# Optimization experiments

Hardware: AMD Instinct MI355X
Metric: run time of the kernel (lower is better)

Reference implementation:

```python
import jax, jax.numpy as jnp
import numpy as np

B, T, F, H, C = 128, 2048, 2, 64, 2
EPS = 1e-5  # BatchNorm eps (eval mode, running stats)


def setup_inputs() -> dict:
    key = jax.random.key(0)
    ks = jax.random.split(key, 23)
    rn = lambda k, s, sc=0.1: jax.random.normal(k, s, jnp.float32) * sc
    return {
        "x": jax.random.normal(ks[0], (B, T, F), jnp.float32),
        "tags": jax.random.randint(ks[1], (B, T), 0, C),
        "cw1": rn(ks[2], (H, F)), "cb1": rn(ks[3], (H,)),
        "cwr": rn(ks[4], (3, H, H)), "cbr": rn(ks[5], (3, H)),
        "bn_g": 1.0 + rn(ks[6], (4, H)), "bn_b": rn(ks[7], (4, H)),
        "bn_m": rn(ks[8], (4, H)),
        "bn_v": 0.5 + jax.random.uniform(ks[9], (4, H), jnp.float32),
        "wih_f": rn(ks[10], (4 * H, H)), "whh_f": rn(ks[11], (4 * H, H)),
        "bih_f": rn(ks[12], (4 * H,)), "bhh_f": rn(ks[13], (4 * H,)),
        "wih_b": rn(ks[14], (4 * H, H)), "whh_b": rn(ks[15], (4 * H, H)),
        "bih_b": rn(ks[16], (4 * H,)), "bhh_b": rn(ks[17], (4 * H,)),
        "fc_w": rn(ks[18], (C, 2 * H)), "fc_b": rn(ks[19], (C,)),
        "crf_start": rn(ks[20], (C,)), "crf_end": rn(ks[21], (C,)),
        "crf_trans": rn(ks[22], (C, C)),
    }


def _block(y, w, b, g, be, m, v):
    # Conv1d(kernel_size=1) == per-timestep linear; GELU (exact erf); eval BatchNorm1d
    y = jnp.einsum('bti,hi->bth', y, w) + b
    y = jax.nn.gelu(y, approximate=False)
    return (y - m) / jnp.sqrt(v + EPS) * g + be


def _lstm(xs, wih, whh, bih, bhh):
    # xs: [T, B, H]; PyTorch gate order i, f, g, o
    h0 = jnp.zeros((xs.shape[1], whh.shape[1]), xs.dtype)

    def step(carry, xt):
        h, c = carry
        z = xt @ wih.T + h @ whh.T + bih + bhh
        i, f, g, o = jnp.split(z, 4, axis=-1)
        c = jax.nn.sigmoid(f) * c + jax.nn.sigmoid(i) * jnp.tanh(g)
        h = jax.nn.sigmoid(o) * jnp.tanh(c)
        return (h, c), h

    _, hs = jax.lax.scan(step, (h0, h0), xs)
    return hs  # [T, B, H]


def reference(x, tags, cw1, cb1, cwr, cbr, bn_g, bn_b, bn_m, bn_v,
              wih_f, whh_f, bih_f, bhh_f, wih_b, whh_b, bih_b, bhh_b,
              fc_w, fc_b, crf_start, crf_end, crf_trans):
    # --- 1x1-conv stack (dropout is identity in eval) ---
    y = _block(x, cw1, cb1, bn_g[0], bn_b[0], bn_m[0], bn_v[0])
    for i in range(3):
        y = _block(y, cwr[i], cbr[i], bn_g[i + 1], bn_b[i + 1], bn_m[i + 1], bn_v[i + 1])
    # --- BiLSTM ---
    xt = jnp.transpose(y, (1, 0, 2))                       # [T, B, H]
    hf = _lstm(xt, wih_f, whh_f, bih_f, bhh_f)
    hb = _lstm(xt[::-1], wih_b, whh_b, bih_b, bhh_b)[::-1]
    h = jnp.concatenate([hf, hb], axis=-1)                 # [T, B, 2H]
    em = jnp.transpose(h @ fc_w.T + fc_b, (1, 0, 2))       # [B, T, C] emissions
    # --- CRF log-partition (forward algorithm, lax.scan over time) ---
    alpha0 = crf_start + em[:, 0]                          # [B, C]

    def step(alpha, et):
        a = jax.scipy.special.logsumexp(alpha[:, :, None] + crf_trans[None], axis=1) + et
        return a, None

    alpha, _ = jax.lax.scan(step, alpha0, jnp.transpose(em[:, 1:], (1, 0, 2)))
    logZ = jax.scipy.special.logsumexp(alpha + crf_end, axis=1)  # [B]
    # --- gold-path score ---
    num = crf_start[tags[:, 0]] + crf_end[tags[:, -1]]
    num = num + jnp.take_along_axis(em, tags[:, :, None], axis=2)[..., 0].sum(axis=1)
    num = num + crf_trans[tags[:, :-1], tags[:, 1:]].sum(axis=1)
    # model returns -crf(logits, tags) with reduction='sum' -> scalar NLL
    return -(num - logZ).sum()
```

## Files before the change

### kernel.cpp

```cpp
#include <hip/hip_runtime.h>
#include <hip/hip_bf16.h>

#define BB 128
#define TT 2048
#define HH 64
#define BT (BB * TT)
#define EPS_BN 1e-5f

typedef unsigned short ushort_t;
typedef short s8v __attribute__((ext_vector_type(8)));
typedef float f4v __attribute__((ext_vector_type(4)));

__device__ __forceinline__ float gelu_exact(float x) {
    return 0.5f * x * (1.0f + erff(x * 0.70710678118654752440f));
}
__device__ __forceinline__ ushort_t f2bf(float v) {
    __hip_bfloat16 h = __float2bfloat16(v);
    return *reinterpret_cast<ushort_t*>(&h);
}
__device__ __forceinline__ float lse2(float a, float b) {
    float m = fmaxf(a, b);
    return m + log1pf(__expf(-fabsf(a - b)));
}

__global__ __launch_bounds__(256, 4) void conv_kernel(
    const float* __restrict__ x, const float* __restrict__ cw1, const float* __restrict__ cb1,
    const float* __restrict__ cwr, const float* __restrict__ cbr,
    const float* __restrict__ bn_g, const float* __restrict__ bn_b,
    const float* __restrict__ bn_m, const float* __restrict__ bn_v,
    ushort_t* __restrict__ y) {
    __shared__ ushort_t s_wc[3 * 64 * 64];
    __shared__ float s_l1[64 * 4];
    __shared__ float s_sc[256], s_sh[256];
    __shared__ float s_cb[192];
    __shared__ ushort_t s_act[4][1024];

    int tid = threadIdx.x;
    for (int i = tid; i < 3 * 64 * 64; i += 256) {
        int row = (i >> 6) & 63, col = i & 63;
        unsigned by = (unsigned)((i >> 6) * 128 + col * 2) ^ (unsigned)((row & 7) << 4);
        s_wc[by >> 1] = f2bf(cwr[i]);
    }
    if (tid < 64) {
        s_l1[tid * 4 + 0] = cw1[tid * 2 + 0];
        s_l1[tid * 4 + 1] = cw1[tid * 2 + 1];
        s_l1[tid * 4 + 2] = cb1[tid];
    }
    if (tid < 256) {
        float sc = bn_g[tid] * rsqrtf(bn_v[tid] + EPS_BN);
        s_sc[tid] = sc;
        s_sh[tid] = bn_b[tid] - bn_m[tid] * sc;
    }
    if (tid < 192) s_cb[tid] = cbr[tid];
    __syncthreads();

    int wid = tid >> 6, l = tid & 63;
    int lrow = l & 15, lgrp = l >> 4;
    ushort_t* act = s_act[wid];
    int gwave = blockIdx.x * 4 + wid;

    for (int strip = gwave; strip < 16384; strip += 4096) {
        int p0 = strip << 4;
        float2 xv = ((const float2*)x)[p0 + lrow];
        s8v fa0, fa1;
#pragma unroll
        for (int j = 0; j < 8; ++j) {
            int c0 = lgrp * 8 + j, c1 = 32 + c0;
            float t0 = s_l1[c0 * 4] * xv.x + s_l1[c0 * 4 + 1] * xv.y + s_l1[c0 * 4 + 2];
            t0 = gelu_exact(t0) * s_sc[c0] + s_sh[c0];
            fa0[j] = (short)f2bf(t0);
            float t1 = s_l1[c1 * 4] * xv.x + s_l1[c1 * 4 + 1] * xv.y + s_l1[c1 * 4 + 2];
            t1 = gelu_exact(t1) * s_sc[c1] + s_sh[c1];
            fa1[j] = (short)f2bf(t1);
        }
#pragma unroll
        for (int L = 0; L < 3; ++L) {
            f4v acc[4];
#pragma unroll
            for (int nt = 0; nt < 4; ++nt) {
                acc[nt] = (f4v){0.f, 0.f, 0.f, 0.f};
                int row = nt * 16 + lrow;
                unsigned b0 = (unsigned)(L * 8192 + row * 128 + lgrp * 16) ^ (unsigned)((row & 7) << 4);
                unsigned b1 = (unsigned)(L * 8192 + row * 128 + lgrp * 16 + 64) ^ (unsigned)((row & 7) << 4);
                s8v fb0 = *(const s8v*)((const char*)s_wc + b0);
                s8v fb1 = *(const s8v*)((const char*)s_wc + b1);
                acc[nt] = __builtin_amdgcn_mfma_f32_16x16x32_bf16(fa0, fb0, acc[nt], 0, 0, 0);
                acc[nt] = __builtin_amdgcn_mfma_f32_16x16x32_bf16(fa1, fb1, acc[nt], 0, 0, 0);
            }
#pragma unroll
            for (int nt = 0; nt < 4; ++nt) {
                int ch = nt * 16 + lrow;
#pragma unroll
                for (int i = 0; i < 4; ++i) {
                    float v = acc[nt][i] + s_cb[L * 64 + ch];
                    v = gelu_exact(v) * s_sc[(L + 1) * 64 + ch] + s_sh[(L + 1) * 64 + ch];
                    int pos = lgrp * 4 + i;
                    unsigned by = (unsigned)(pos * 128 + ch * 2) ^ (unsigned)((pos & 7) << 4);
                    *(ushort_t*)((char*)act + by) = f2bf(v);
                }
            }
            if (L < 2) {
                unsigned r0 = (unsigned)(lrow * 128 + lgrp * 16) ^ (unsigned)((lrow & 7) << 4);
                unsigned r1 = (unsigned)(lrow * 128 + lgrp * 16 + 64) ^ (unsigned)((lrow & 7) << 4);
                fa0 = *(const s8v*)((const char*)act + r0);
                fa1 = *(const s8v*)((const char*)act + r1);
            }
        }
        int prow = l >> 2, pc = l & 3;
        unsigned so0 = (unsigned)(prow * 128 + pc * 32) ^ (unsigned)((prow & 7) << 4);
        unsigned so1 = (unsigned)(prow * 128 + pc * 32 + 16) ^ (unsigned)((prow & 7) << 4);
        s8v v0 = *(const s8v*)((const char*)act + so0);
        s8v v1 = *(const s8v*)((const char*)act + so1);
        char* yb = (char*)y + (size_t)(p0 + prow) * 128 + pc * 32;
        *(s8v*)yb = v0;
        *(s8v*)(yb + 16) = v1;
    }
}

__device__ __forceinline__ unsigned ring_addr(int slot, int bb, int ub) {
    return (unsigned)(slot * 2048) + (((unsigned)(bb * 128 + ub)) ^ ((unsigned)((bb & 7) << 4)));
}

template <int PAR>
__device__ __forceinline__ void lstm_strip(
    int s, int w, int lb, int lg, int b, int d, int t0, int dstep,
    const s8v (&whhA)[4][2], const s8v (&wihA)[4][2],
    const f4v (&zbias)[4], const s8v (&femA)[2],
    const s8v (&ybCur)[4][2], s8v (&ybNxt)[4][2],
    float (&cst)[4], ushort_t* ring,
    const char* __restrict__ ybase, float2* __restrict__ emv) {
    f4v zin[4][4];
#pragma unroll
    for (int g = 0; g < 4; ++g)
#pragma unroll
        for (int ct = 0; ct < 4; ++ct) {
            f4v a = zbias[g];
            a = __builtin_amdgcn_mfma_f32_16x16x32_bf16(wihA[g][0], ybCur[ct][0], a, 0, 0, 0);
            a = __builtin_amdgcn_mfma_f32_16x16x32_bf16(wihA[g][1], ybCur[ct][1], a, 0, 0, 0);
            zin[g][ct] = a;
        }
    if (s + 1 < 512) {
#pragma unroll
        for (int ct = 0; ct < 4; ++ct) {
            int t = t0 + dstep * ((s + 1) * 4 + ct);
            const char* p = ybase + (size_t)t * 128 + lg * 16;
            ybNxt[ct][0] = *(const s8v*)p;
            ybNxt[ct][1] = *(const s8v*)(p + 64);
        }
    }
    if (w == 0 && s > 0) {
#pragma unroll
        for (int ct = 0; ct < 4; ++ct) {
            int slot = (1 - PAR) * 4 + ct;
            s8v hlo = *(const s8v*)((const char*)ring + ring_addr(slot, lb, lg * 16));
            s8v hhi = *(const s8v*)((const char*)ring + ring_addr(slot, lb, 64 + lg * 16));
            f4v a = (f4v){0.f, 0.f, 0.f, 0.f};
            a = __builtin_amdgcn_mfma_f32_16x16x32_bf16(femA[0], hlo, a, 0, 0, 0);
            a = __builtin_amdgcn_mfma_f32_16x16x32_bf16(femA[1], hhi, a, 0, 0, 0);
            if (lg == 0) {
                int t = t0 + dstep * ((s - 1) * 4 + ct);
                emv[((size_t)d * TT + t) * BB + b] = make_float2(a[0], a[1]);
            }
        }
    }
#pragma unroll
    for (int j = 0; j < 4; ++j) {
        const int prev = (j == 0) ? ((1 - PAR) * 4 + 3) : (PAR * 4 + j - 1);
        const int slot = PAR * 4 + j;
        s8v hlo = *(const s8v*)((const char*)ring + ring_addr(prev, lb, lg * 16));
        s8v hhi = *(const s8v*)((const char*)ring + ring_addr(prev, lb, 64 + lg * 16));
        f4v a0 = __builtin_amdgcn_mfma_f32_16x16x32_bf16(whhA[0][0], hlo, zin[0][j], 0, 0, 0);
        f4v a1 = __builtin_amdgcn_mfma_f32_16x16x32_bf16(whhA[1][0], hlo, zin[1][j], 0, 0, 0);
        f4v a2 = __builtin_amdgcn_mfma_f32_16x16x32_bf16(whhA[2][0], hlo, zin[2][j], 0, 0, 0);
        f4v a3 = __builtin_amdgcn_mfma_f32_16x16x32_bf16(whhA[3][0], hlo, zin[3][j], 0, 0, 0);
        a0 = __builtin_amdgcn_mfma_f32_16x16x32_bf16(whhA[0][1], hhi, a0, 0, 0, 0);
        a1 = __builtin_amdgcn_mfma_f32_16x16x32_bf16(whhA[1][1], hhi, a1, 0, 0, 0);
        a2 = __builtin_amdgcn_mfma_f32_16x16x32_bf16(whhA[2][1], hhi, a2, 0, 0, 0);
        a3 = __builtin_amdgcn_mfma_f32_16x16x32_bf16(whhA[3][1], hhi, a3, 0, 0, 0);
        unsigned hp0 = 0, hp1 = 0;
#pragma unroll
        for (int i = 0; i < 4; ++i) {
            float zi = a0[i], zf = a1[i], zg = a2[i], zo = a3[i];
            float ig = 1.f / (1.f + __expf(-zi));
            float fg = 1.f / (1.f + __expf(-zf));
            float gg = 1.f - 2.f / (__expf(2.f * zg) + 1.f);
            float og = 1.f / (1.f + __expf(-zo));
            float cn = fg * cst[i] + ig * gg;
            cst[i] = cn;
            float th = 1.f - 2.f / (__expf(2.f * cn) + 1.f);
            unsigned hb_ = (unsigned)f2bf(og * th);
            if (i == 0) hp0 = hb_;
            else if (i == 1) hp0 |= hb_ << 16;
            else if (i == 2) hp1 = hb_;
            else hp1 |= hb_ << 16;
        }
        *(uint2*)((char*)ring + ring_addr(slot, lb, (16 * w + lg * 4) * 2)) = make_uint2(hp0, hp1);
        __syncthreads();
    }
}

__global__ __launch_bounds__(256, 1) void lstm_kernel(
    const ushort_t* __restrict__ y,
    const float* __restrict__ whh_f, const float* __restrict__ whh_b,
    const float* __restrict__ wih_f, const float* __restrict__ wih_b,
    const float* __restrict__ bih_f, const float* __restrict__ bhh_f,
    const float* __restrict__ bih_b, const float* __restrict__ bhh_b,
    const float* __restrict__ fc_w, float* __restrict__ em_ws) {
    __shared__ ushort_t ring[8 * 1024];
    int d = blockIdx.x >> 3, bg = blockIdx.x & 7;
    const float* whh = d ? whh_b : whh_f;
    const float* wih = d ? wih_b : wih_f;
    const float* bih = d ? bih_b : bih_f;
    const float* bhh = d ? bhh_b : bhh_f;
    int tid = threadIdx.x;
    int w = tid >> 6, l = tid & 63, lb = l & 15, lg = l >> 4;
    int b = bg * 16 + lb;

    for (int i = tid; i < 4096; i += 256) ((unsigned*)ring)[i] = 0u;

    s8v whhA[4][2], wihA[4][2];
#pragma unroll
    for (int g = 0; g < 4; ++g)
#pragma unroll
        for (int kh = 0; kh < 2; ++kh) {
            s8v va, vb;
#pragma unroll
            for (int j = 0; j < 8; ++j) {
                int row = g * 64 + 16 * w + lb;
                int k = kh * 32 + lg * 8 + j;
                va[j] = (short)f2bf(whh[(size_t)row * 64 + k]);
                vb[j] = (short)f2bf(wih[(size_t)row * 64 + k]);
            }
            whhA[g][kh] = va;
            wihA[g][kh] = vb;
        }
    f4v zbias[4];
#pragma unroll
    for (int g = 0; g < 4; ++g)
#pragma unroll
        for (int i = 0; i < 4; ++i) {
            int u = 16 * w + lg * 4 + i;
            zbias[g][i] = bih[g * 64 + u] + bhh[g * 64 + u];
        }
    s8v femA[2];
#pragma unroll
    for (int kh = 0; kh < 2; ++kh)
#pragma unroll
        for (int j = 0; j < 8; ++j) {
            int k = kh * 32 + lg * 8 + j;
            femA[kh][j] = (lb < 2) ? (short)f2bf(fc_w[lb * 128 + d * 64 + k]) : (short)0;
        }

    int t0 = d ? (TT - 1) : 0;
    int dstep = d ? -1 : 1;
    const char* ybase = (const char*)y + (size_t)b * TT * 128;
    float2* emv = (float2*)em_ws;

    s8v ybA[4][2], ybB[4][2];
#pragma unroll
    for (int ct = 0; ct < 4; ++ct) {
        int t = t0 + dstep * ct;
        const char* p = ybase + (size_t)t * 128 + lg * 16;
        ybA[ct][0] = *(const s8v*)p;
        ybA[ct][1] = *(const s8v*)(p + 64);
    }
    float cst[4] = {0.f, 0.f, 0.f, 0.f};
    __syncthreads();

    for (int sp = 0; sp < 256; ++sp) {
        lstm_strip<0>(2 * sp, w, lb, lg, b, d, t0, dstep, whhA, wihA, zbias, femA,
                      ybA, ybB, cst, ring, ybase, emv);
        lstm_strip<1>(2 * sp + 1, w, lb, lg, b, d, t0, dstep, whhA, wihA, zbias, femA,
                      ybB, ybA, cst, ring, ybase, emv);
    }
    if (w == 0) {
#pragma unroll
        for (int ct = 0; ct < 4; ++ct) {
            int slot = 4 + ct;
            s8v hlo = *(const s8v*)((const char*)ring + ring_addr(slot, lb, lg * 16));
            s8v hhi = *(const s8v*)((const char*)ring + ring_addr(slot, lb, 64 + lg * 16));
            f4v a = (f4v){0.f, 0.f, 0.f, 0.f};
            a = __builtin_amdgcn_mfma_f32_16x16x32_bf16(femA[0], hlo, a, 0, 0, 0);
            a = __builtin_amdgcn_mfma_f32_16x16x32_bf16(femA[1], hhi, a, 0, 0, 0);
            if (lg == 0) {
                int t = t0 + dstep * (511 * 4 + ct);
                emv[((size_t)d * TT + t) * BB + b] = make_float2(a[0], a[1]);
            }
        }
    }
}

__global__ __launch_bounds__(128) void crf_kernel(
    const float* __restrict__ em_ws, const int* __restrict__ tags,
    const float* __restrict__ fc_b, const float* __restrict__ crf_start,
    const float* __restrict__ crf_end, const float* __restrict__ crf_trans,
    float* __restrict__ nll_ws) {
    int b = blockIdx.x, c = threadIdx.x;
    float fb0 = fc_b[0], fb1 = fc_b[1];
    float t00 = crf_trans[0], t01 = crf_trans[1], t10 = crf_trans[2], t11 = crf_trans[3];
    const float2* p0 = (const float2*)em_ws;
    const float2* p1 = p0 + (size_t)TT * BB;
    const int* tg = tags + (size_t)b * TT;

    int tbeg = 1 + 16 * c;
    int tend = min(TT, tbeg + 16);
    float P00, P01, P10, P11;
    float np = 0.f;
    int tprev = tg[tbeg - 1];
    {
        float2 ea = p0[(size_t)tbeg * BB + b], eb = p1[(size_t)tbeg * BB + b];
        float e0 = ea.x + eb.x + fb0, e1 = ea.y + eb.y + fb1;
        P00 = t00 + e0; P01 = t01 + e1; P10 = t10 + e0; P11 = t11 + e1;
        int tc = tg[tbeg];
        np += (tc ? e1 : e0) + (tprev ? (tc ? t11 : t10) : (tc ? t01 : t00));
        tprev = tc;
    }
    for (int t = tbeg + 1; t < tend; ++t) {
        float2 ea = p0[(size_t)t * BB + b], eb = p1[(size_t)t * BB + b];
        float e0 = ea.x + eb.x + fb0, e1 = ea.y + eb.y + fb1;
        float n00 = lse2(P00 + t00, P01 + t10) + e0;
        float n01 = lse2(P00 + t01, P01 + t11) + e1;
        float n10 = lse2(P10 + t00, P11 + t10) + e0;
        float n11 = lse2(P10 + t01, P11 + t11) + e1;
        P00 = n00; P01 = n01; P10 = n10; P11 = n11;
        int tc = tg[t];
        np += (tc ? e1 : e0) + (tprev ? (tc ? t11 : t10) : (tc ? t01 : t00));
        tprev = tc;
    }
    __shared__ float sP[128][4];
    __shared__ float sN[128];
    sP[c][0] = P00; sP[c][1] = P01; sP[c][2] = P10; sP[c][3] = P11;
    sN[c] = np;
    __syncthreads();
    if (c == 0) {
        float2 ea = p0[b], eb = p1[b];
        float e0 = ea.x + eb.x + fb0, e1 = ea.y + eb.y + fb1;
        float a0 = crf_start[0] + e0, a1 = crf_start[1] + e1;
        float num = tg[0] ? (crf_start[1] + e1) : (crf_start[0] + e0);
        for (int k = 0; k < 128; ++k) {
            float q0 = lse2(a0 + sP[k][0], a1 + sP[k][2]);
            float q1 = lse2(a0 + sP[k][1], a1 + sP[k][3]);
            a0 = q0; a1 = q1;
            num += sN[k];
        }
        num += crf_end[tg[TT - 1]];
        float logZ = lse2(a0 + crf_end[0], a1 + crf_end[1]);
        nll_ws[b] = logZ - num;
    }
}

__global__ __launch_bounds__(128) void sum_kernel(const float* __restrict__ nll_ws,
                                                  float* __restrict__ out) {
    __shared__ float red[BB];
    red[threadIdx.x] = nll_ws[threadIdx.x];
    __syncthreads();
    if (threadIdx.x == 0) {
        float s = 0.f;
        for (int i = 0; i < BB; ++i) s += red[i];
        out[0] = s;
    }
}

extern "C" void kernel_launch(void* const* d_in, const int* in_sizes, int n_in,
                              void* d_out, int out_size, void* d_ws, size_t ws_size,
                              hipStream_t stream) {
    const float* x = (const float*)d_in[0];
    const int* tags = (const int*)d_in[1];
    const float* cw1 = (const float*)d_in[2];
    const float* cb1 = (const float*)d_in[3];
    const float* cwr = (const float*)d_in[4];
    const float* cbr = (const float*)d_in[5];
    const float* bn_g = (const float*)d_in[6];
    const float* bn_b = (const float*)d_in[7];
    const float* bn_m = (const float*)d_in[8];
    const float* bn_v = (const float*)d_in[9];
    const float* wih_f = (const float*)d_in[10];
    const float* whh_f = (const float*)d_in[11];
    const float* bih_f = (const float*)d_in[12];
    const float* bhh_f = (const float*)d_in[13];
    const float* wih_b = (const float*)d_in[14];
    const float* whh_b = (const float*)d_in[15];
    const float* bih_b = (const float*)d_in[16];
    const float* bhh_b = (const float*)d_in[17];
    const float* fc_w = (const float*)d_in[18];
    const float* fc_b = (const float*)d_in[19];
    const float* crf_start = (const float*)d_in[20];
    const float* crf_end = (const float*)d_in[21];
    const float* crf_trans = (const float*)d_in[22];
    float* out = (float*)d_out;

    ushort_t* y = (ushort_t*)d_ws;
    float* em = (float*)((char*)d_ws + (size_t)BT * 64 * 2);
    float* nll = (float*)((char*)d_ws + (size_t)BT * 64 * 2 + (size_t)2 * TT * BB * 2 * 4);

    conv_kernel<<<1024, 256, 0, stream>>>(x, cw1, cb1, cwr, cbr, bn_g, bn_b, bn_m, bn_v, y);
    lstm_kernel<<<16, 256, 0, stream>>>(y, whh_f, whh_b, wih_f, wih_b,
                                        bih_f, bhh_f, bih_b, bhh_b, fc_w, em);
    crf_kernel<<<128, 128, 0, stream>>>(em, tags, fc_b, crf_start, crf_end, crf_trans, nll);
    sum_kernel<<<1, 128, 0, stream>>>(nll, out);
}
```

Before: 2.199 ms.

## Restructure LSTM to one batch element per single-wave block

The LSTM kernel changes from 16 four-wave blocks, each covering 16 batch elements with MFMA and a block barrier every timestep, to 256 single-wave blocks that each handle one (direction, batch) pair. The recurrent matvec now runs as fp32 FMAs against W_hh held in registers. h is exchanged through an LDS ring inside one wavefront, so no __syncthreads is needed. The input projection is batched over 16 timesteps with MFMA against W_ih staged in LDS, and the emission projection runs once per strip. This aims to spread the serial recurrence across many more CUs and drop the per-step cross-wave barrier, at the cost of heavy register use and a longer scalar FMA chain per step.

```diff
diff --git a/kernel.cpp b/kernel.cpp
--- a/kernel.cpp
+++ b/kernel.cpp
@@ -117,175 +117,144 @@
     }
 }
 
-__device__ __forceinline__ unsigned ring_addr(int slot, int bb, int ub) {
-    return (unsigned)(slot * 2048) + (((unsigned)(bb * 128 + ub)) ^ ((unsigned)((bb & 7) << 4)));
-}
-
-template <int PAR>
-__device__ __forceinline__ void lstm_strip(
-    int s, int w, int lb, int lg, int b, int d, int t0, int dstep,
-    const s8v (&whhA)[4][2], const s8v (&wihA)[4][2],
-    const f4v (&zbias)[4], const s8v (&femA)[2],
-    const s8v (&ybCur)[4][2], s8v (&ybNxt)[4][2],
-    float (&cst)[4], ushort_t* ring,
-    const char* __restrict__ ybase, float2* __restrict__ emv) {
-    f4v zin[4][4];
-#pragma unroll
-    for (int g = 0; g < 4; ++g)
-#pragma unroll
-        for (int ct = 0; ct < 4; ++ct) {
-            f4v a = zbias[g];
-            a = __builtin_amdgcn_mfma_f32_16x16x32_bf16(wihA[g][0], ybCur[ct][0], a, 0, 0, 0);
-            a = __builtin_amdgcn_mfma_f32_16x16x32_bf16(wihA[g][1], ybCur[ct][1], a, 0, 0, 0);
-            zin[g][ct] = a;
-        }
-    if (s + 1 < 512) {
-#pragma unroll
-        for (int ct = 0; ct < 4; ++ct) {
-            int t = t0 + dstep * ((s + 1) * 4 + ct);
-            const char* p = ybase + (size_t)t * 128 + lg * 16;
-            ybNxt[ct][0] = *(const s8v*)p;
-            ybNxt[ct][1] = *(const s8v*)(p + 64);
-        }
-    }
-    if (w == 0 && s > 0) {
-#pragma unroll
-        for (int ct = 0; ct < 4; ++ct) {
-            int slot = (1 - PAR) * 4 + ct;
-            s8v hlo = *(const s8v*)((const char*)ring + ring_addr(slot, lb, lg * 16));
-            s8v hhi = *(const s8v*)((const char*)ring + ring_addr(slot, lb, 64 + lg * 16));
-            f4v a = (f4v){0.f, 0.f, 0.f, 0.f};
-            a = __builtin_amdgcn_mfma_f32_16x16x32_bf16(femA[0], hlo, a, 0, 0, 0);
-            a = __builtin_amdgcn_mfma_f32_16x16x32_bf16(femA[1], hhi, a, 0, 0, 0);
-            if (lg == 0) {
-                int t = t0 + dstep * ((s - 1) * 4 + ct);
-                emv[((size_t)d * TT + t) * BB + b] = make_float2(a[0], a[1]);
-            }
-        }
-    }
-#pragma unroll
-    for (int j = 0; j < 4; ++j) {
-        const int prev = (j == 0) ? ((1 - PAR) * 4 + 3) : (PAR * 4 + j - 1);
-        const int slot = PAR * 4 + j;
-        s8v hlo = *(const s8v*)((const char*)ring + ring_addr(prev, lb, lg * 16));
-        s8v hhi = *(const s8v*)((const char*)ring + ring_addr(prev, lb, 64 + lg * 16));
-        f4v a0 = __builtin_amdgcn_mfma_f32_16x16x32_bf16(whhA[0][0], hlo, zin[0][j], 0, 0, 0);
-        f4v a1 = __builtin_amdgcn_mfma_f32_16x16x32_bf16(whhA[1][0], hlo, zin[1][j], 0, 0, 0);
-        f4v a2 = __builtin_amdgcn_mfma_f32_16x16x32_bf16(whhA[2][0], hlo, zin[2][j], 0, 0, 0);
-        f4v a3 = __builtin_amdgcn_mfma_f32_16x16x32_bf16(whhA[3][0], hlo, zin[3][j], 0, 0, 0);
-        a0 = __builtin_amdgcn_mfma_f32_16x16x32_bf16(whhA[0][1], hhi, a0, 0, 0, 0);
-        a1 = __builtin_amdgcn_mfma_f32_16x16x32_bf16(whhA[1][1], hhi, a1, 0, 0, 0);
-        a2 = __builtin_amdgcn_mfma_f32_16x16x32_bf16(whhA[2][1], hhi, a2, 0, 0, 0);
-        a3 = __builtin_amdgcn_mfma_f32_16x16x32_bf16(whhA[3][1], hhi, a3, 0, 0, 0);
-        unsigned hp0 = 0, hp1 = 0;
-#pragma unroll
-        for (int i = 0; i < 4; ++i) {
-            float zi = a0[i], zf = a1[i], zg = a2[i], zo = a3[i];
-            float ig = 1.f / (1.f + __expf(-zi));
-            float fg = 1.f / (1.f + __expf(-zf));
-            float gg = 1.f - 2.f / (__expf(2.f * zg) + 1.f);
-            float og = 1.f / (1.f + __expf(-zo));
-            float cn = fg * cst[i] + ig * gg;
-            cst[i] = cn;
-            float th = 1.f - 2.f / (__expf(2.f * cn) + 1.f);
-            unsigned hb_ = (unsigned)f2bf(og * th);
-            if (i == 0) hp0 = hb_;
-            else if (i == 1) hp0 |= hb_ << 16;
-            else if (i == 2) hp1 = hb_;
-            else hp1 |= hb_ << 16;
-        }
-        *(uint2*)((char*)ring + ring_addr(slot, lb, (16 * w + lg * 4) * 2)) = make_uint2(hp0, hp1);
-        __syncthreads();
-    }
-}
-
-__global__ __launch_bounds__(256, 1) void lstm_kernel(
+__global__ __launch_bounds__(64, 1) void lstm_kernel(
     const ushort_t* __restrict__ y,
     const float* __restrict__ whh_f, const float* __restrict__ whh_b,
     const float* __restrict__ wih_f, const float* __restrict__ wih_b,
     const float* __restrict__ bih_f, const float* __restrict__ bhh_f,
     const float* __restrict__ bih_b, const float* __restrict__ bhh_b,
     const float* __restrict__ fc_w, float* __restrict__ em_ws) {
-    __shared__ ushort_t ring[8 * 1024];
-    int d = blockIdx.x >> 3, bg = blockIdx.x & 7;
+    __shared__ ushort_t s_wih[256 * 64];
+    __shared__ float zlds[16][260];
+    __shared__ float ring[32][72];
+    __shared__ ushort_t embuf[2][16][72];
+
+    int bid = blockIdx.x;
+    int d = bid >> 7, b = bid & 127;
     const float* whh = d ? whh_b : whh_f;
     const float* wih = d ? wih_b : wih_f;
     const float* bih = d ? bih_b : bih_f;
     const float* bhh = d ? bhh_b : bhh_f;
-    int tid = threadIdx.x;
-    int w = tid >> 6, l = tid & 63, lb = l & 15, lg = l >> 4;
-    int b = bg * 16 + lb;
-
-    for (int i = tid; i < 4096; i += 256) ((unsigned*)ring)[i] = 0u;
-
-    s8v whhA[4][2], wihA[4][2];
-#pragma unroll
-    for (int g = 0; g < 4; ++g)
-#pragma unroll
-        for (int kh = 0; kh < 2; ++kh) {
-            s8v va, vb;
-#pragma unroll
-            for (int j = 0; j < 8; ++j) {
-                int row = g * 64 + 16 * w + lb;
-                int k = kh * 32 + lg * 8 + j;
-                va[j] = (short)f2bf(whh[(size_t)row * 64 + k]);
-                vb[j] = (short)f2bf(wih[(size_t)row * 64 + k]);
-            }
-            whhA[g][kh] = va;
-            wihA[g][kh] = vb;
-        }
-    f4v zbias[4];
-#pragma unroll
-    for (int g = 0; g < 4; ++g)
-#pragma unroll
-        for (int i = 0; i < 4; ++i) {
-            int u = 16 * w + lg * 4 + i;
-            zbias[g][i] = bih[g * 64 + u] + bhh[g * 64 + u];
-        }
-    s8v femA[2];
-#pragma unroll
-    for (int kh = 0; kh < 2; ++kh)
-#pragma unroll
-        for (int j = 0; j < 8; ++j) {
-            int k = kh * 32 + lg * 8 + j;
-            femA[kh][j] = (lb < 2) ? (short)f2bf(fc_w[lb * 128 + d * 64 + k]) : (short)0;
-        }
+
+    int l = threadIdx.x;
+    int lc = l & 15, lg = l >> 4;
+
+    for (int i = l; i < 256 * 64; i += 64) {
+        int r = i >> 6, k = i & 63, u = r >> 2, g = r & 3;
+        unsigned by = (unsigned)(r * 128 + k * 2) ^ (unsigned)((r & 7) << 4);
+        s_wih[by >> 1] = f2bf(wih[(size_t)(g * 64 + u) * 64 + k]);
+    }
+    for (int i = l; i < 32 * 72; i += 64) (&ring[0][0])[i] = 0.f;
+
+    float4 wr0[16], wr1[16], wr2[16], wr3[16];
+#pragma unroll
+    for (int m = 0; m < 16; ++m) {
+        wr0[m] = *(const float4*)(whh + (size_t)(0 * 64 + l) * 64 + m * 4);
+        wr1[m] = *(const float4*)(whh + (size_t)(1 * 64 + l) * 64 + m * 4);
+        wr2[m] = *(const float4*)(whh + (size_t)(2 * 64 + l) * 64 + m * 4);
+        wr3[m] = *(const float4*)(whh + (size_t)(3 * 64 + l) * 64 + m * 4);
+    }
+    float4 zb;
+    zb.x = bih[0 * 64 + l] + bhh[0 * 64 + l];
+    zb.y = bih[1 * 64 + l] + bhh[1 * 64 + l];
+    zb.z = bih[2 * 64 + l] + bhh[2 * 64 + l];
+    zb.w = bih[3 * 64 + l] + bhh[3 * 64 + l];
+
+    s8v femA0, femA1;
+#pragma unroll
+    for (int j = 0; j < 8; ++j) {
+        femA0[j] = (lc < 2) ? (short)f2bf(fc_w[lc * 128 + d * 64 + lg * 8 + j]) : (short)0;
+        femA1[j] = (lc < 2) ? (short)f2bf(fc_w[lc * 128 + d * 64 + 32 + lg * 8 + j]) : (short)0;
+    }
 
     int t0 = d ? (TT - 1) : 0;
     int dstep = d ? -1 : 1;
     const char* ybase = (const char*)y + (size_t)b * TT * 128;
     float2* emv = (float2*)em_ws;
 
-    s8v ybA[4][2], ybB[4][2];
-#pragma unroll
-    for (int ct = 0; ct < 4; ++ct) {
-        int t = t0 + dstep * ct;
+    s8v yc0, yc1;
+    {
+        int t = t0 + dstep * lc;
         const char* p = ybase + (size_t)t * 128 + lg * 16;
-        ybA[ct][0] = *(const s8v*)p;
-        ybA[ct][1] = *(const s8v*)(p + 64);
-    }
-    float cst[4] = {0.f, 0.f, 0.f, 0.f};
-    __syncthreads();
-
-    for (int sp = 0; sp < 256; ++sp) {
-        lstm_strip<0>(2 * sp, w, lb, lg, b, d, t0, dstep, whhA, wihA, zbias, femA,
-                      ybA, ybB, cst, ring, ybase, emv);
-        lstm_strip<1>(2 * sp + 1, w, lb, lg, b, d, t0, dstep, whhA, wihA, zbias, femA,
-                      ybB, ybA, cst, ring, ybase, emv);
-    }
-    if (w == 0) {
-#pragma unroll
-        for (int ct = 0; ct < 4; ++ct) {
-            int slot = 4 + ct;
-            s8v hlo = *(const s8v*)((const char*)ring + ring_addr(slot, lb, lg * 16));
-            s8v hhi = *(const s8v*)((const char*)ring + ring_addr(slot, lb, 64 + lg * 16));
+        yc0 = *(const s8v*)p;
+        yc1 = *(const s8v*)(p + 64);
+    }
+    float cst = 0.f;
+
+    for (int sp = 0; sp < 128; ++sp) {
+#pragma unroll
+        for (int n = 0; n < 16; ++n) {
+            int r = 16 * n + lc;
+            unsigned a0b = (unsigned)(r * 128 + lg * 16) ^ (unsigned)((r & 7) << 4);
+            unsigned a1b = (unsigned)(r * 128 + lg * 16 + 64) ^ (unsigned)((r & 7) << 4);
+            s8v fb0 = *(const s8v*)((const char*)s_wih + a0b);
+            s8v fb1 = *(const s8v*)((const char*)s_wih + a1b);
+            f4v acc = (f4v){0.f, 0.f, 0.f, 0.f};
+            acc = __builtin_amdgcn_mfma_f32_16x16x32_bf16(fb0, yc0, acc, 0, 0, 0);
+            acc = __builtin_amdgcn_mfma_f32_16x16x32_bf16(fb1, yc1, acc, 0, 0, 0);
+            *(float4*)&zlds[lc][(4 * n + lg) * 4] = make_float4(acc[0], acc[1], acc[2], acc[3]);
+        }
+        if (sp > 0) {
+            const ushort_t* eb = &embuf[(sp - 1) & 1][0][0];
+            s8v hb0 = *(const s8v*)((const char*)eb + lc * 144 + lg * 16);
+            s8v hb1 = *(const s8v*)((const char*)eb + lc * 144 + lg * 16 + 64);
             f4v a = (f4v){0.f, 0.f, 0.f, 0.f};
-            a = __builtin_amdgcn_mfma_f32_16x16x32_bf16(femA[0], hlo, a, 0, 0, 0);
-            a = __builtin_amdgcn_mfma_f32_16x16x32_bf16(femA[1], hhi, a, 0, 0, 0);
+            a = __builtin_amdgcn_mfma_f32_16x16x32_bf16(femA0, hb0, a, 0, 0, 0);
+            a = __builtin_amdgcn_mfma_f32_16x16x32_bf16(femA1, hb1, a, 0, 0, 0);
             if (lg == 0) {
-                int t = t0 + dstep * (511 * 4 + ct);
+                int t = t0 + dstep * ((sp - 1) * 16 + lc);
                 emv[((size_t)d * TT + t) * BB + b] = make_float2(a[0], a[1]);
             }
+        }
+        s8v yn0 = yc0, yn1 = yc1;
+        if (sp + 1 < 128) {
+            int t = t0 + dstep * ((sp + 1) * 16 + lc);
+            const char* p = ybase + (size_t)t * 128 + lg * 16;
+            yn0 = *(const s8v*)p;
+            yn1 = *(const s8v*)(p + 64);
+        }
+        for (int j = 0; j < 16; ++j) {
+            int prev = (j == 0) ? ((((sp & 1) ^ 1) << 4) + 15) : (((sp & 1) << 4) + j - 1);
+            float4 hh[16];
+#pragma unroll
+            for (int m = 0; m < 16; ++m) hh[m] = *(const float4*)&ring[prev][m * 4];
+            float a0 = 0.f, a1 = 0.f, a2 = 0.f, a3 = 0.f;
+#pragma unroll
+            for (int m = 0; m < 16; ++m) {
+                float4 h4 = hh[m];
+                a0 += h4.x * wr0[m].x + h4.y * wr0[m].y + h4.z * wr0[m].z + h4.w * wr0[m].w;
+                a1 += h4.x * wr1[m].x + h4.y * wr1[m].y + h4.z * wr1[m].z + h4.w * wr1[m].w;
+                a2 += h4.x * wr2[m].x + h4.y * wr2[m].y + h4.z * wr2[m].z + h4.w * wr2[m].w;
+                a3 += h4.x * wr3[m].x + h4.y * wr3[m].y + h4.z * wr3[m].z + h4.w * wr3[m].w;
+            }
+            float4 z4 = *(const float4*)&zlds[j][l * 4];
+            a0 += z4.x + zb.x;
+            a1 += z4.y + zb.y;
+            a2 += z4.z + zb.z;
+            a3 += z4.w + zb.w;
+            float ig = 1.f / (1.f + __expf(-a0));
+            float fg = 1.f / (1.f + __expf(-a1));
+            float gg = 1.f - 2.f / (__expf(2.f * a2) + 1.f);
+            float og = 1.f / (1.f + __expf(-a3));
+            cst = fg * cst + ig * gg;
+            float h = og * (1.f - 2.f / (__expf(2.f * cst) + 1.f));
+            int slot = ((sp & 1) << 4) + j;
+            ring[slot][l] = h;
+            embuf[sp & 1][j][l] = f2bf(h);
+        }
+        yc0 = yn0;
+        yc1 = yn1;
+    }
+    {
+        const ushort_t* eb = &embuf[1][0][0];
+        s8v hb0 = *(const s8v*)((const char*)eb + lc * 144 + lg * 16);
+        s8v hb1 = *(const s8v*)((const char*)eb + lc * 144 + lg * 16 + 64);
+        f4v a = (f4v){0.f, 0.f, 0.f, 0.f};
+        a = __builtin_amdgcn_mfma_f32_16x16x32_bf16(femA0, hb0, a, 0, 0, 0);
+        a = __builtin_amdgcn_mfma_f32_16x16x32_bf16(femA1, hb1, a, 0, 0, 0);
+        if (lg == 0) {
+            int t = t0 + dstep * (127 * 16 + lc);
+            emv[((size_t)d * TT + t) * BB + b] = make_float2(a[0], a[1]);
         }
     }
 }
@@ -394,7 +363,7 @@
     float* nll = (float*)((char*)d_ws + (size_t)BT * 64 * 2 + (size_t)2 * TT * BB * 2 * 4);
 
     conv_kernel<<<1024, 256, 0, stream>>>(x, cw1, cb1, cwr, cbr, bn_g, bn_b, bn_m, bn_v, y);
-    lstm_kernel<<<16, 256, 0, stream>>>(y, whh_f, whh_b, wih_f, wih_b,
+    lstm_kernel<<<256, 64, 0, stream>>>(y, whh_f, whh_b, wih_f, wih_b,
                                         bih_f, bhh_f, bih_b, bhh_b, fc_w, em);
     crf_kernel<<<128, 128, 0, stream>>>(em, tags, fc_b, crf_start, crf_end, crf_trans, nll);
     sum_kernel<<<1, 128, 0, stream>>>(nll, out);
```

Result: slower. 2.443 ms (+11.1%).
